# Performance work log

Measured on AMD Instinct MI355X. Metric: run time of the kernel, lower is better.

Reference implementation:

```python
import jax, jax.numpy as jnp
import numpy as np

B, N, HD = 4, 2048, 256
E, T = 4096, 1024
PROPAG_STEPS = 5
ALPHA_MAX = 0.2
LN_EPS = 1e-5


def setup_inputs() -> dict:
    key = jax.random.key(0)
    ks = jax.random.split(key, 16)
    s_in, s_h = (2.0 * HD) ** -0.5, HD ** -0.5
    return {
        "attr_matrix": jax.random.normal(ks[0], (B, N, 1), dtype=jnp.float32),
        "adj_matrix": jax.random.uniform(ks[1], (B, N, N), dtype=jnp.float32),
        # ggnn.linear_i: 1 -> HD
        "W_i": jax.random.normal(ks[2], (HD, 1), dtype=jnp.float32),
        "b_i": jnp.zeros((HD,), dtype=jnp.float32),
        # ggnn.gru: GRUCell(input=2*HD, hidden=HD), torch gate order r,z,n
        "W_ih": jax.random.normal(ks[3], (3 * HD, 2 * HD), dtype=jnp.float32) * s_in,
        "b_ih": jnp.zeros((3 * HD,), dtype=jnp.float32),
        "W_hh": jax.random.normal(ks[4], (3 * HD, HD), dtype=jnp.float32) * s_h,
        "b_hh": jnp.zeros((3 * HD,), dtype=jnp.float32),
        # ggnn.linear_o: HD -> 1
        "W_o": jax.random.normal(ks[5], (1, HD), dtype=jnp.float32) * s_h,
        "b_o": jnp.zeros((1,), dtype=jnp.float32),
        # topo buffers (incidence-like, kept small to mimic sparse +/-1 matrices)
        "B1": jax.random.normal(ks[6], (N, E), dtype=jnp.float32) * 0.02,
        "B2": jax.random.normal(ks[7], (E, T), dtype=jnp.float32) * 0.02,
        # topo trainables
        "proj_W": jax.random.normal(ks[8], (HD, HD), dtype=jnp.float32) * s_h,
        "ln_gamma": jnp.ones((HD,), dtype=jnp.float32),
        "ln_beta": jnp.zeros((HD,), dtype=jnp.float32),
        "alpha_raw": jnp.float32(-2.0),
    }


def _gru_cell(x, h, W_ih, b_ih, W_hh, b_hh):
    # x: [B,N,2H], h: [B,N,H]; torch GRUCell gate order: r, z, n
    gx = jnp.einsum('bni,gi->bng', x, W_ih) + b_ih
    gh = jnp.einsum('bnh,gh->bng', h, W_hh) + b_hh
    xr, xz, xn = jnp.split(gx, 3, axis=-1)
    hr, hz, hn = jnp.split(gh, 3, axis=-1)
    r = jax.nn.sigmoid(xr + hr)
    z = jax.nn.sigmoid(xz + hz)
    n = jnp.tanh(xn + r * hn)
    return (1.0 - z) * n + z * h


def _layernorm(x, gamma, beta):
    mu = jnp.mean(x, axis=-1, keepdims=True)
    var = jnp.mean(jnp.square(x - mu), axis=-1, keepdims=True)
    return (x - mu) * jax.lax.rsqrt(var + LN_EPS) * gamma + beta


def reference(attr_matrix, adj_matrix, W_i, b_i, W_ih, b_ih, W_hh, b_hh,
              W_o, b_o, B1, B2, proj_W, ln_gamma, ln_beta, alpha_raw):
    A_in = adj_matrix                      # [B,N,N]
    A_out = jnp.swapaxes(adj_matrix, -2, -1)
    # linear_i + relu
    h = jax.nn.relu(jnp.einsum('bnc,hc->bnh', attr_matrix, W_i) + b_i)  # [B,N,H]
    # GGNN propagation
    for _ in range(PROPAG_STEPS):
        a_in = jnp.einsum('bnm,bmh->bnh', A_in, h)
        a_out = jnp.einsum('bnm,bmh->bnh', A_out, h)
        h = _gru_cell(jnp.concatenate((a_in, a_out), axis=-1), h,
                      W_ih, b_ih, W_hh, b_hh)
    # topo residual: dH = B1 (L1 (B1^T h)), L1 = B1^T B1 + B2 B2^T
    L1 = B1.T @ B1 + B2 @ B2.T             # [E,E]
    E_feat = jnp.einsum('ne,bnh->beh', B1, h)       # B1^T H
    E_topo = jnp.einsum('ef,bfh->beh', L1, E_feat)
    dH = jnp.einsum('ne,beh->bnh', B1, E_topo)
    dH = _layernorm(jax.nn.relu(jnp.einsum('bnh,oh->bno', dH, proj_W)),
                    ln_gamma, ln_beta)
    alpha = ALPHA_MAX * jax.nn.sigmoid(alpha_raw)
    h = h + alpha * dH
    # linear_o -> [B,N] (squeeze(0) is a no-op for B>1)
    anomaly = (jnp.einsum('bnh,oh->bno', h, W_o) + b_o)[..., 0]
    return anomaly
```

## Files before the change

### kernel.cpp

```cpp
#include <hip/hip_runtime.h>
#include <hip/hip_fp16.h>


typedef __bf16 bf16x8 __attribute__((ext_vector_type(8)));
typedef _Float16 f16x8 __attribute__((ext_vector_type(8)));
typedef float f32x4 __attribute__((ext_vector_type(4)));

#define BM 128
#define BN 128
#define BK 16
#define LO_INV (1.f / 1024.f)

__device__ __forceinline__ unsigned short bf16rne(float x)
{
    unsigned u = __float_as_uint(x);
    return (unsigned short)((u + 0x7FFFu + ((u >> 16) & 1u)) >> 16);
}
__device__ __forceinline__ float bf2f(unsigned short h)
{
    return __uint_as_float((unsigned)h << 16);
}
__device__ __forceinline__ void split2(float x, unsigned short& hi, unsigned short& lo)
{
    hi = bf16rne(x);
    lo = bf16rne(x - bf2f(hi));
}

__device__ __forceinline__ unsigned short f16r(float x)
{
    return __half_as_ushort(__float2half(x));
}
__device__ __forceinline__ float f16f(unsigned short u)
{
    return __half2float(__ushort_as_half(u));
}
__device__ __forceinline__ void splitf(float x, unsigned short& hi, unsigned short& lo)
{
    hi = f16r(x);
    lo = f16r((x - f16f(hi)) * 1024.f);
}

__device__ __forceinline__ void gload_lds16(const unsigned short* g, unsigned short* l)
{
    __builtin_amdgcn_global_load_lds(
        (const __attribute__((address_space(1))) void*)g,
        (__attribute__((address_space(3))) void*)l, 16, 0, 0);
}

__device__ __forceinline__ void stage2(const unsigned short* g, unsigned short* l, int K)
{
    gload_lds16(g, l);
    gload_lds16(g + (size_t)32 * K, l + 2048);
}

template<int SPLIT>
__device__ __forceinline__ void mm_loop64f(
    const unsigned short* ag0, const unsigned short* ag1,
    const unsigned short* bg0, const unsigned short* bg1,
    int K, unsigned short* LDS, int tid,
    f32x4 (&acc0)[2][2], f32x4 (&acc1)[2][2])
{
    constexpr int NT = SPLIT ? 2 : 1;
    constexpr int TSZ = 4096;

    int lane = tid & 63, r16 = lane & 15, g = lane >> 4, s7 = r16 & 7;
    int wv = tid >> 6, wr = wv >> 1, wc = wv & 1;
    int arow = (wr * 32 + r16) * 128;
    int brow = (wc * 32 + r16) * 128;
    unsigned short* lA = LDS + (tid >> 6) * 512;
    unsigned short* lB = LDS + NT * TSZ + (tid >> 6) * 512;
    const char* Ab = (const char*)LDS;
    const char* Bb = (const char*)(LDS + NT * TSZ);

    for (int k0 = 0; k0 < K; k0 += 64) {
        stage2(ag0 + k0, lA, K);
        if constexpr (SPLIT) stage2(ag1 + k0, lA + TSZ, K);
        stage2(bg0 + k0, lB, K);
        if constexpr (SPLIT) stage2(bg1 + k0, lB + TSZ, K);
        __syncthreads();
#pragma unroll
        for (int ks = 0; ks < 2; ++ks) {
            int tt = ((ks * 4 + g) ^ s7) * 16;
            f16x8 a0[2], a1[2], b0[2], b1[2];
#pragma unroll
            for (int mi = 0; mi < 2; ++mi) {
                a0[mi] = *(const f16x8*)(Ab + arow + mi * 2048 + tt);
                if constexpr (SPLIT)
                    a1[mi] = *(const f16x8*)(Ab + TSZ * 2 + arow + mi * 2048 + tt);
            }
#pragma unroll
            for (int ni = 0; ni < 2; ++ni) {
                b0[ni] = *(const f16x8*)(Bb + brow + ni * 2048 + tt);
                if constexpr (SPLIT)
                    b1[ni] = *(const f16x8*)(Bb + TSZ * 2 + brow + ni * 2048 + tt);
            }
#pragma unroll
            for (int mi = 0; mi < 2; ++mi)
#pragma unroll
                for (int ni = 0; ni < 2; ++ni) {
                    if constexpr (SPLIT) {
                        acc1[mi][ni] = __builtin_amdgcn_mfma_f32_16x16x32_f16(
                            a1[mi], b0[ni], acc1[mi][ni], 0, 0, 0);
                        acc1[mi][ni] = __builtin_amdgcn_mfma_f32_16x16x32_f16(
                            a0[mi], b1[ni], acc1[mi][ni], 0, 0, 0);
                    }
                    acc0[mi][ni] = __builtin_amdgcn_mfma_f32_16x16x32_f16(
                        a0[mi], b0[ni], acc0[mi][ni], 0, 0, 0);
                }
        }
        __syncthreads();
    }
}

template<int SPLIT, int OF16>
__global__ __launch_bounds__(256, 2) void mm_f16(
    const unsigned short* __restrict__ Ah, const unsigned short* __restrict__ Al,
    const unsigned short* __restrict__ Bh, const unsigned short* __restrict__ Bl,
    int K, const float* __restrict__ bias, const float* __restrict__ Cacc,
    void* __restrict__ Cout, int ldc)
{
    constexpr int NT = SPLIT ? 2 : 1;
    __shared__ unsigned short LDS[2 * NT * 4096];
    int tid = threadIdx.x;

    unsigned nwg = gridDim.x * gridDim.y;
    unsigned lin = blockIdx.y * gridDim.x + blockIdx.x;
    unsigned wk = ((nwg & 7) == 0) ? (lin & 7) * (nwg >> 3) + (lin >> 3) : lin;
    unsigned bx = wk % gridDim.x, by = wk / gridDim.x;

    int m0 = by * 64, n0 = bx * 64;
    int rp = tid >> 3, sl8 = ((tid & 7) ^ (rp & 7)) * 8;
    const unsigned short* ag0 = Ah + (size_t)(m0 + rp) * K + sl8;
    const unsigned short* ag1 = SPLIT ? Al + (size_t)(m0 + rp) * K + sl8 : nullptr;
    const unsigned short* bg0 = Bh + (size_t)(n0 + rp) * K + sl8;
    const unsigned short* bg1 = SPLIT ? Bl + (size_t)(n0 + rp) * K + sl8 : nullptr;

    f32x4 acc0[2][2], acc1[2][2];
#pragma unroll
    for (int mi = 0; mi < 2; ++mi)
#pragma unroll
        for (int ni = 0; ni < 2; ++ni) {
            acc0[mi][ni] = (f32x4){0.f, 0.f, 0.f, 0.f};
            acc1[mi][ni] = (f32x4){0.f, 0.f, 0.f, 0.f};
        }

    mm_loop64f<SPLIT>(ag0, ag1, bg0, bg1, K, LDS, tid, acc0, acc1);

    int lane = tid & 63, r16 = lane & 15, g = lane >> 4;
    int wv = tid >> 6, wr = wv >> 1, wc = wv & 1;
#pragma unroll
    for (int mi = 0; mi < 2; ++mi) {
#pragma unroll
        for (int ni = 0; ni < 2; ++ni) {
            int col = n0 + wc * 32 + ni * 16 + r16;
            float badd = bias ? bias[col] : 0.f;
#pragma unroll
            for (int j = 0; j < 4; ++j) {
                int row = m0 + wr * 32 + mi * 16 + g * 4 + j;
                float v = acc0[mi][ni][j] + badd;
                if (SPLIT) v += acc1[mi][ni][j] * LO_INV;
                if (Cacc) v += Cacc[(size_t)row * ldc + col];
                if (OF16)
                    ((unsigned short*)Cout)[(size_t)row * ldc + col] = f16r(v);
                else
                    ((float*)Cout)[(size_t)row * ldc + col] = v;
            }
        }
    }
}

__global__ __launch_bounds__(256, 2) void mm_step1f(
    const unsigned short* __restrict__ AhHi, const unsigned short* __restrict__ AhLo,
    const unsigned short* __restrict__ AtHi, const unsigned short* __restrict__ AtLo,
    const unsigned short* __restrict__ hTh, const unsigned short* __restrict__ hTl,
    unsigned short* __restrict__ Xhi, unsigned short* __restrict__ Xlo,
    const unsigned short* __restrict__ hrmh, const unsigned short* __restrict__ hrml,
    const unsigned short* __restrict__ WhhH, const unsigned short* __restrict__ WhhL,
    const float* __restrict__ b_hh, float* __restrict__ ghb)
{
    __shared__ unsigned short LDS[16384];
    int tid = threadIdx.x;
    unsigned bid = blockIdx.x;
    int lane = tid & 63, r16 = lane & 15, g = lane >> 4;
    int wv = tid >> 6, wr = wv >> 1, wc = wv & 1;
    int rp = tid >> 3, sl8 = ((tid & 7) ^ (rp & 7)) * 8;

    f32x4 acc0[2][2], acc1[2][2];
#pragma unroll
    for (int mi = 0; mi < 2; ++mi)
#pragma unroll
        for (int ni = 0; ni < 2; ++ni) {
            acc0[mi][ni] = (f32x4){0.f, 0.f, 0.f, 0.f};
            acc1[mi][ni] = (f32x4){0.f, 0.f, 0.f, 0.f};
        }

    if (bid < 1024) {
        unsigned wk = (bid & 7) * 128 + (bid >> 3);
        unsigned bz = wk >> 7, rem = wk & 127, by = rem >> 2, bx = rem & 3;
        int b = bz >> 1, wio = bz & 1;
        const unsigned short* Ahp = (wio ? AtHi : AhHi) + (size_t)b * 4194304;
        const unsigned short* Alp = (wio ? AtLo : AhLo) + (size_t)b * 4194304;
        size_t boff = (size_t)(b * 256 + bx * 64) * 2048;
        int m0 = by * 64;
        const int K = 2048;
        const unsigned short* ag0 = Ahp + (size_t)(m0 + rp) * K + sl8;
        const unsigned short* ag1 = Alp + (size_t)(m0 + rp) * K + sl8;
        const unsigned short* bg0 = hTh + boff + (size_t)rp * K + sl8;
        const unsigned short* bg1 = hTl + boff + (size_t)rp * K + sl8;

        mm_loop64f<1>(ag0, ag1, bg0, bg1, K, LDS, tid, acc0, acc1);

        float* T = reinterpret_cast<float*>(LDS);
#pragma unroll
        for (int mi = 0; mi < 2; ++mi)
#pragma unroll
            for (int ni = 0; ni < 2; ++ni)
#pragma unroll
                for (int j = 0; j < 4; ++j)
                    T[(wr * 32 + mi * 16 + g * 4 + j) * 68 +
                      wc * 32 + ni * 16 + r16] =
                        acc0[mi][ni][j] + acc1[mi][ni][j] * LO_INV;
        __syncthreads();

        int row = tid >> 2, fq = tid & 3;
        const float* src = T + row * 68 + fq * 16;
        unsigned hw[8], lw[8];
#pragma unroll
        for (int e = 0; e < 8; ++e) {
            unsigned short h0, l0, h1, l1;
            splitf(src[2 * e], h0, l0);
            splitf(src[2 * e + 1], h1, l1);
            hw[e] = (unsigned)h0 | ((unsigned)h1 << 16);
            lw[e] = (unsigned)l0 | ((unsigned)l1 << 16);
        }
        size_t base = ((size_t)(m0 + row) * 4 + b) * 512 + wio * 256 + bx * 64 + fq * 16;
        ((uint4*)(Xhi + base))[0] = (uint4){hw[0], hw[1], hw[2], hw[3]};
        ((uint4*)(Xhi + base))[1] = (uint4){hw[4], hw[5], hw[6], hw[7]};
        ((uint4*)(Xlo + base))[0] = (uint4){lw[0], lw[1], lw[2], lw[3]};
        ((uint4*)(Xlo + base))[1] = (uint4){lw[4], lw[5], lw[6], lw[7]};
    } else {
        unsigned gidx = bid - 1024;
        unsigned by = gidx / 12, bx = gidx % 12;
        int m0 = by * 64, n0 = bx * 64;
        const int K = 256;
        const unsigned short* ag0 = hrmh + (size_t)(m0 + rp) * K + sl8;
        const unsigned short* ag1 = hrml + (size_t)(m0 + rp) * K + sl8;
        const unsigned short* bg0 = WhhH + (size_t)(n0 + rp) * K + sl8;
        const unsigned short* bg1 = WhhL + (size_t)(n0 + rp) * K + sl8;

        mm_loop64f<1>(ag0, ag1, bg0, bg1, K, LDS, tid, acc0, acc1);

#pragma unroll
        for (int mi = 0; mi < 2; ++mi) {
#pragma unroll
            for (int ni = 0; ni < 2; ++ni) {
                int col = n0 + wc * 32 + ni * 16 + r16;
                float badd = b_hh[col];
#pragma unroll
                for (int j = 0; j < 4; ++j) {
                    int row = m0 + wr * 32 + mi * 16 + g * 4 + j;
                    ghb[(size_t)row * 768 + col] =
                        acc0[mi][ni][j] + acc1[mi][ni][j] * LO_INV + badd;
                }
            }
        }
    }
}

__global__ void split_adj16(const float* __restrict__ adj,
                            unsigned short* __restrict__ nhi, unsigned short* __restrict__ nlo,
                            unsigned short* __restrict__ thi, unsigned short* __restrict__ tlo)
{
    __shared__ float t[64][68];
    int z = blockIdx.z;
    const float* src = adj + (size_t)z * 4194304;
    int tx = threadIdx.x & 15, ty = threadIdx.x >> 4;
    int i0 = blockIdx.y * 64, j0 = blockIdx.x * 64;
#pragma unroll
    for (int i = 0; i < 4; ++i) {
        int r = ty * 4 + i;
        float4 v = *(const float4*)(src + (size_t)(i0 + r) * 2048 + j0 + tx * 4);
        ushort4 h, l;
        splitf(v.x, h.x, l.x); splitf(v.y, h.y, l.y);
        splitf(v.z, h.z, l.z); splitf(v.w, h.w, l.w);
        size_t o = (size_t)z * 4194304 + (size_t)(i0 + r) * 2048 + j0 + tx * 4;
        *(ushort4*)(nhi + o) = h; *(ushort4*)(nlo + o) = l;
        t[r][tx * 4 + 0] = v.x; t[r][tx * 4 + 1] = v.y;
        t[r][tx * 4 + 2] = v.z; t[r][tx * 4 + 3] = v.w;
    }
    __syncthreads();
#pragma unroll
    for (int i = 0; i < 4; ++i) {
        int r = ty * 4 + i;
        ushort4 h, l;
        splitf(t[tx * 4 + 0][r], h.x, l.x);
        splitf(t[tx * 4 + 1][r], h.y, l.y);
        splitf(t[tx * 4 + 2][r], h.z, l.z);
        splitf(t[tx * 4 + 3][r], h.w, l.w);
        size_t o = (size_t)z * 4194304 + (size_t)(j0 + r) * 2048 + i0 + tx * 4;
        *(ushort4*)(thi + o) = h; *(ushort4*)(tlo + o) = l;
    }
}

__global__ void split_h16(const float* __restrict__ h,
                          unsigned short* __restrict__ hi, unsigned short* __restrict__ lo,
                          unsigned short* __restrict__ hrmh, unsigned short* __restrict__ hrml)
{
    __shared__ float t[64][68];
    int f0 = blockIdx.x * 64, n0 = blockIdx.y * 64;
    int tx = threadIdx.x & 15, ty = threadIdx.x >> 4;
#pragma unroll
    for (int i = 0; i < 4; ++i) {
        int r = ty * 4 + i;
        float4 v = *(const float4*)(h + (size_t)(n0 + r) * 1024 + f0 + tx * 4);
        t[r][tx * 4 + 0] = v.x; t[r][tx * 4 + 1] = v.y;
        t[r][tx * 4 + 2] = v.z; t[r][tx * 4 + 3] = v.w;
        if (hrmh) {
            ushort4 hh, ll;
            splitf(v.x, hh.x, ll.x); splitf(v.y, hh.y, ll.y);
            splitf(v.z, hh.z, ll.z); splitf(v.w, hh.w, ll.w);
            size_t o = (size_t)(n0 + r) * 1024 + f0 + tx * 4;
            *(ushort4*)(hrmh + o) = hh;
            *(ushort4*)(hrml + o) = ll;
        }
    }
    __syncthreads();
#pragma unroll
    for (int i = 0; i < 4; ++i) {
        int r = ty * 4 + i;
        ushort4 hh, ll;
        splitf(t[tx * 4 + 0][r], hh.x, ll.x);
        splitf(t[tx * 4 + 1][r], hh.y, ll.y);
        splitf(t[tx * 4 + 2][r], hh.z, ll.z);
        splitf(t[tx * 4 + 3][r], hh.w, ll.w);
        size_t o = (size_t)(f0 + r) * 2048 + n0 + tx * 4;
        *(ushort4*)(hi + o) = hh; *(ushort4*)(lo + o) = ll;
    }
}

__global__ void split_t16(const float* __restrict__ in, unsigned short* __restrict__ outN,
                          unsigned short* __restrict__ outT, int R, int C)
{
    __shared__ float t[64][68];
    int i0 = blockIdx.y * 64, j0 = blockIdx.x * 64;
    int tx = threadIdx.x & 15, ty = threadIdx.x >> 4;
#pragma unroll
    for (int i = 0; i < 4; ++i) {
        int r = ty * 4 + i;
        float4 v = *(const float4*)(in + (size_t)(i0 + r) * C + j0 + tx * 4);
        ushort4 hh;
        hh.x = f16r(v.x); hh.y = f16r(v.y);
        hh.z = f16r(v.z); hh.w = f16r(v.w);
        *(ushort4*)(outN + (size_t)(i0 + r) * C + j0 + tx * 4) = hh;
        t[r][tx * 4 + 0] = v.x; t[r][tx * 4 + 1] = v.y;
        t[r][tx * 4 + 2] = v.z; t[r][tx * 4 + 3] = v.w;
    }
    __syncthreads();
#pragma unroll
    for (int i = 0; i < 4; ++i) {
        int r = ty * 4 + i;
        ushort4 hh;
        hh.x = f16r(t[tx * 4 + 0][r]);
        hh.y = f16r(t[tx * 4 + 1][r]);
        hh.z = f16r(t[tx * 4 + 2][r]);
        hh.w = f16r(t[tx * 4 + 3][r]);
        *(ushort4*)(outT + (size_t)(j0 + r) * R + i0 + tx * 4) = hh;
    }
}

__global__ void split_w16(const float* __restrict__ Wih, const float* __restrict__ Whh,
                          const float* __restrict__ pj,
                          unsigned short* __restrict__ WihH, unsigned short* __restrict__ WihL,
                          unsigned short* __restrict__ WhhH, unsigned short* __restrict__ WhhL,
                          unsigned short* __restrict__ pjH)
{
    int i = blockIdx.x * 256 + threadIdx.x;
    if (i < 393216) {
        unsigned short h, l;
        splitf(Wih[i], h, l);
        WihH[i] = h; WihL[i] = l;
    } else if (i < 589824) {
        int j = i - 393216;
        unsigned short h, l;
        splitf(Whh[j], h, l);
        WhhH[j] = h; WhhL[j] = l;
    } else if (i < 655360) {
        int j = i - 589824;
        pjH[j] = f16r(pj[j]);
    }
}

__global__ __launch_bounds__(256, 2) void gemm_f32(
    const float* __restrict__ A, const float* __restrict__ B, float* __restrict__ C,
    int M, int N, int K, int lda, int ldb, int ldc,
    long sA, long sB, long sC,
    const float* __restrict__ bias, int ta, int tb, int accum)
{
    int bz = blockIdx.z;
    int taEff = ta;
    if (ta == 2) {
        int b = bz >> 1, w = bz & 1;
        A += (long)b * sA; B += (long)b * sB; C += (long)b * sC + w * 256;
        taEff = w;
    } else {
        A += (long)bz * sA; B += (long)bz * sB; C += (long)bz * sC;
    }
    int m0 = blockIdx.y * BM, n0 = blockIdx.x * BN;

    __shared__ float As[BK][BM + 4];
    __shared__ float Bs[BK][BN + 4];

    int tid = threadIdx.x;
    int tx = tid & 15, ty = tid >> 4;

    float acc[64];
#pragma unroll
    for (int i = 0; i < 64; ++i) acc[i] = 0.f;

    for (int k0 = 0; k0 < K; k0 += BK) {
        if (!taEff) {
            int m = tid >> 1, kk = (tid & 1) * 8;
            const float* src = A + (long)(m0 + m) * lda + (k0 + kk);
            float4 v0 = *(const float4*)(src);
            float4 v1 = *(const float4*)(src + 4);
            As[kk + 0][m] = v0.x; As[kk + 1][m] = v0.y;
            As[kk + 2][m] = v0.z; As[kk + 3][m] = v0.w;
            As[kk + 4][m] = v1.x; As[kk + 5][m] = v1.y;
            As[kk + 6][m] = v1.z; As[kk + 7][m] = v1.w;
        } else {
            int k = tid >> 4, mm = (tid & 15) * 8;
            const float* src = A + (long)(k0 + k) * lda + (m0 + mm);
            *(float4*)&As[k][mm]     = *(const float4*)(src);
            *(float4*)&As[k][mm + 4] = *(const float4*)(src + 4);
        }
        if (!tb) {
            int k = tid >> 4, nn = (tid & 15) * 8;
            const float* src = B + (long)(k0 + k) * ldb + (n0 + nn);
            *(float4*)&Bs[k][nn]     = *(const float4*)(src);
            *(float4*)&Bs[k][nn + 4] = *(const float4*)(src + 4);
        } else {
            int n = tid >> 1, kk = (tid & 1) * 8;
            const float* src = B + (long)(n0 + n) * ldb + (k0 + kk);
            float4 v0 = *(const float4*)(src);
            float4 v1 = *(const float4*)(src + 4);
            Bs[kk + 0][n] = v0.x; Bs[kk + 1][n] = v0.y;
            Bs[kk + 2][n] = v0.z; Bs[kk + 3][n] = v0.w;
            Bs[kk + 4][n] = v1.x; Bs[kk + 5][n] = v1.y;
            Bs[kk + 6][n] = v1.z; Bs[kk + 7][n] = v1.w;
        }
        __syncthreads();

#pragma unroll
        for (int k = 0; k < BK; ++k) {
            float a[8], b[8];
            *(float4*)&a[0] = *(const float4*)&As[k][ty * 4];
            *(float4*)&a[4] = *(const float4*)&As[k][64 + ty * 4];
            *(float4*)&b[0] = *(const float4*)&Bs[k][tx * 4];
            *(float4*)&b[4] = *(const float4*)&Bs[k][64 + tx * 4];
#pragma unroll
            for (int i = 0; i < 8; ++i)
#pragma unroll
                for (int j = 0; j < 8; ++j)
                    acc[i * 8 + j] += a[i] * b[j];
        }
        __syncthreads();
    }

#pragma unroll
    for (int i = 0; i < 8; ++i) {
        int row = m0 + ((i >> 2) ? 64 : 0) + ty * 4 + (i & 3);
#pragma unroll
        for (int jh = 0; jh < 2; ++jh) {
            int col = n0 + jh * 64 + tx * 4;
            float4 v;
            v.x = acc[i * 8 + jh * 4 + 0];
            v.y = acc[i * 8 + jh * 4 + 1];
            v.z = acc[i * 8 + jh * 4 + 2];
            v.w = acc[i * 8 + jh * 4 + 3];
            if (bias) {
                v.x += bias[col + 0]; v.y += bias[col + 1];
                v.z += bias[col + 2]; v.w += bias[col + 3];
            }
            float* dst = C + (long)row * ldc + col;
            if (accum) {
                float4 o = *(const float4*)dst;
                v.x += o.x; v.y += o.y; v.z += o.z; v.w += o.w;
            }
            *(float4*)dst = v;
        }
    }
}

__global__ void split_adj(const float* __restrict__ adj,
                          unsigned short* __restrict__ nhi, unsigned short* __restrict__ nlo,
                          unsigned short* __restrict__ thi, unsigned short* __restrict__ tlo)
{
    __shared__ float t[64][68];
    int z = blockIdx.z;
    const float* src = adj + (size_t)z * 4194304;
    int tx = threadIdx.x & 15, ty = threadIdx.x >> 4;
    int i0 = blockIdx.y * 64, j0 = blockIdx.x * 64;
#pragma unroll
    for (int i = 0; i < 4; ++i) {
        int r = ty * 4 + i;
        float4 v = *(const float4*)(src + (size_t)(i0 + r) * 2048 + j0 + tx * 4);
        ushort4 h, l;
        split2(v.x, h.x, l.x); split2(v.y, h.y, l.y);
        split2(v.z, h.z, l.z); split2(v.w, h.w, l.w);
        size_t o = (size_t)z * 4194304 + (size_t)(i0 + r) * 2048 + j0 + tx * 4;
        *(ushort4*)(nhi + o) = h; *(ushort4*)(nlo + o) = l;
        t[r][tx * 4 + 0] = v.x; t[r][tx * 4 + 1] = v.y;
        t[r][tx * 4 + 2] = v.z; t[r][tx * 4 + 3] = v.w;
    }
    __syncthreads();
#pragma unroll
    for (int i = 0; i < 4; ++i) {
        int r = ty * 4 + i;
        ushort4 h, l;
        split2(t[tx * 4 + 0][r], h.x, l.x);
        split2(t[tx * 4 + 1][r], h.y, l.y);
        split2(t[tx * 4 + 2][r], h.z, l.z);
        split2(t[tx * 4 + 3][r], h.w, l.w);
        size_t o = (size_t)z * 4194304 + (size_t)(j0 + r) * 2048 + i0 + tx * 4;
        *(ushort4*)(thi + o) = h; *(ushort4*)(tlo + o) = l;
    }
}

__global__ void split_h(const float* __restrict__ h,
                        unsigned short* __restrict__ hi, unsigned short* __restrict__ lo)
{
    __shared__ float t[64][68];
    int f0 = blockIdx.x * 64, n0 = blockIdx.y * 64;
    int tx = threadIdx.x & 15, ty = threadIdx.x >> 4;
#pragma unroll
    for (int i = 0; i < 4; ++i) {
        int r = ty * 4 + i;
        float4 v = *(const float4*)(h + (size_t)(n0 + r) * 1024 + f0 + tx * 4);
        t[r][tx * 4 + 0] = v.x; t[r][tx * 4 + 1] = v.y;
        t[r][tx * 4 + 2] = v.z; t[r][tx * 4 + 3] = v.w;
    }
    __syncthreads();
#pragma unroll
    for (int i = 0; i < 4; ++i) {
        int r = ty * 4 + i;
        ushort4 hh, ll;
        split2(t[tx * 4 + 0][r], hh.x, ll.x);
        split2(t[tx * 4 + 1][r], hh.y, ll.y);
        split2(t[tx * 4 + 2][r], hh.z, ll.z);
        split2(t[tx * 4 + 3][r], hh.w, ll.w);
        size_t o = (size_t)(f0 + r) * 2048 + n0 + tx * 4;
        *(ushort4*)(hi + o) = hh; *(ushort4*)(lo + o) = ll;
    }
}

__global__ __launch_bounds__(256, 3) void adj_mfma(
    const unsigned short* __restrict__ AhHi, const unsigned short* __restrict__ AhLo,
    const unsigned short* __restrict__ AtHi, const unsigned short* __restrict__ AtLo,
    const unsigned short* __restrict__ hTHi, const unsigned short* __restrict__ hTLo,
    float* __restrict__ c0, float* __restrict__ c1, float* __restrict__ c2)
{
    __shared__ unsigned short As[8192];
    __shared__ unsigned short Bs[8192];
    int tid = threadIdx.x;
    int bz = blockIdx.z;
    int region = bz >> 3, bw = bz & 7, b = bw >> 1, w = bw & 1;
    const unsigned short* Abase =
        (region == 2) ? (w ? AtLo : AhLo) : (w ? AtHi : AhHi);
    Abase += (size_t)b * 4194304;
    const unsigned short* Bbase = (region == 1) ? hTLo : hTHi;
    float* Cb = (region == 0) ? c0 : (region == 1 ? c1 : c2);

    int m0 = blockIdx.y * 128;
    int f0 = b * 256 + blockIdx.x * 128;

    int rp = tid >> 3;
    int sl = (tid & 7) ^ (rp & 7);
    const unsigned short* ag = Abase + (size_t)(m0 + rp) * 2048 + sl * 8;
    const unsigned short* bg = Bbase + (size_t)(f0 + rp) * 2048 + sl * 8;
    unsigned short* al = &As[(tid >> 6) * 512];
    unsigned short* bl = &Bs[(tid >> 6) * 512];

    int lane = tid & 63, r16 = lane & 15, g = lane >> 4;
    int wv = tid >> 6, wr = wv >> 1, wc = wv & 1;
    int s7 = r16 & 7;
    int t0 = (g ^ s7) * 16, t1 = ((4 + g) ^ s7) * 16;
    int arow = (wr * 64 + r16) * 128;
    int brow = (wc * 64 + r16) * 128;

    f32x4 acc[4][4];
#pragma unroll
    for (int mi = 0; mi < 4; ++mi)
#pragma unroll
        for (int ni = 0; ni < 4; ++ni)
            acc[mi][ni] = (f32x4){0.f, 0.f, 0.f, 0.f};

    for (int k0 = 0; k0 < 2048; k0 += 64) {
#pragma unroll
        for (int i = 0; i < 4; ++i)
            gload_lds16(ag + k0 + (size_t)i * 65536, al + i * 2048);
#pragma unroll
        for (int i = 0; i < 4; ++i)
            gload_lds16(bg + k0 + (size_t)i * 65536, bl + i * 2048);
        __syncthreads();

#pragma unroll
        for (int ks = 0; ks < 2; ++ks) {
            int tt = ks ? t1 : t0;
            bf16x8 af[4], bf[4];
#pragma unroll
            for (int mi = 0; mi < 4; ++mi)
                af[mi] = *(const bf16x8*)((const char*)As + arow + mi * 2048 + tt);
#pragma unroll
            for (int ni = 0; ni < 4; ++ni)
                bf[ni] = *(const bf16x8*)((const char*)Bs + brow + ni * 2048 + tt);
#pragma unroll
            for (int mi = 0; mi < 4; ++mi)
#pragma unroll
                for (int ni = 0; ni < 4; ++ni)
                    acc[mi][ni] = __builtin_amdgcn_mfma_f32_16x16x32_bf16(
                        af[mi], bf[ni], acc[mi][ni], 0, 0, 0);
        }
        __syncthreads();
    }

    int cbase = b * 512 + w * 256 + blockIdx.x * 128 + wc * 64;
#pragma unroll
    for (int mi = 0; mi < 4; ++mi) {
        int row = m0 + wr * 64 + mi * 16 + g * 4;
#pragma unroll
        for (int ni = 0; ni < 4; ++ni) {
            int col = cbase + ni * 16 + r16;
            float* dst = Cb + (size_t)row * 2048 + col;
#pragma unroll
            for (int j = 0; j < 4; ++j) dst[(size_t)j * 2048] = acc[mi][ni][j];
        }
    }
}

__global__ void reduce3(float4* __restrict__ x, const float4* __restrict__ p,
                        const float4* __restrict__ q)
{
    int i = blockIdx.x * 256 + threadIdx.x;
    float4 a = x[i], b = p[i], c = q[i];
    a.x += b.x + c.x; a.y += b.y + c.y; a.z += b.z + c.z; a.w += b.w + c.w;
    x[i] = a;
}

__global__ void init_h(const float* __restrict__ attr, const float* __restrict__ W_i,
                       const float* __restrict__ b_i, float* __restrict__ h)
{
    int n = blockIdx.x, b = blockIdx.y, t = threadIdx.x;
    float a = attr[b * 2048 + n];
    h[(long)n * 1024 + b * 256 + t] = fmaxf(a * W_i[t] + b_i[t], 0.f);
}

__global__ void gru_ew(const float* __restrict__ gx, const float* __restrict__ gh,
                       float* __restrict__ h)
{
    int n = blockIdx.x, b = blockIdx.y, t = threadIdx.x;
    long row = ((long)n * 4 + b) * 768;
    float xr = gx[row + t], xz = gx[row + 256 + t], xn = gx[row + 512 + t];
    float hr = gh[row + t], hz = gh[row + 256 + t], hn = gh[row + 512 + t];
    float r = 1.f / (1.f + __expf(-(xr + hr)));
    float z = 1.f / (1.f + __expf(-(xz + hz)));
    float nn = tanhf(xn + r * hn);
    long hi = (long)n * 1024 + b * 256 + t;
    float ho = h[hi];
    h[hi] = (1.f - z) * nn + z * ho;
}

__global__ void ln_out(const float* __restrict__ dP, const float* __restrict__ gamma,
                       const float* __restrict__ beta, const float* __restrict__ araw,
                       const float* __restrict__ h, const float* __restrict__ W_o,
                       const float* __restrict__ b_o, float* __restrict__ out)
{
    int n = blockIdx.x, b = blockIdx.y, t = threadIdx.x;
    long row = ((long)n * 4 + b) * 256;
    float v = fmaxf(dP[row + t], 0.f);
    float s = v, s2 = v * v;
#pragma unroll
    for (int o = 1; o < 64; o <<= 1) { s += __shfl_xor(s, o); s2 += __shfl_xor(s2, o); }
    __shared__ float red[8];
    int w = t >> 6, lane = t & 63;
    if (lane == 0) { red[w] = s; red[4 + w] = s2; }
    __syncthreads();
    float S  = red[0] + red[1] + red[2] + red[3];
    float S2 = red[4] + red[5] + red[6] + red[7];
    float mu = S * (1.f / 256.f);
    float var = S2 * (1.f / 256.f) - mu * mu;
    float rs = rsqrtf(var + 1e-5f);
    float alpha = 0.2f / (1.f + __expf(-araw[0]));
    float y = h[(long)n * 1024 + b * 256 + t] +
              alpha * ((v - mu) * rs * gamma[t] + beta[t]);
    float d = y * W_o[t];
#pragma unroll
    for (int o = 1; o < 64; o <<= 1) d += __shfl_xor(d, o);
    __syncthreads();
    if (lane == 0) red[w] = d;
    __syncthreads();
    if (t == 0) out[(long)b * 2048 + n] = red[0] + red[1] + red[2] + red[3] + b_o[0];
}

__global__ void ln_residual(const float* __restrict__ dP, const float* __restrict__ gamma,
                            const float* __restrict__ beta, const float* __restrict__ araw,
                            float* __restrict__ h)
{
    int n = blockIdx.x, b = blockIdx.y, t = threadIdx.x;
    long row = ((long)n * 4 + b) * 256;
    float v = fmaxf(dP[row + t], 0.f);
    float s = v, s2 = v * v;
#pragma unroll
    for (int o = 1; o < 64; o <<= 1) { s += __shfl_xor(s, o); s2 += __shfl_xor(s2, o); }
    __shared__ float red[8];
    int w = t >> 6, lane = t & 63;
    if (lane == 0) { red[w] = s; red[4 + w] = s2; }
    __syncthreads();
    float S  = red[0] + red[1] + red[2] + red[3];
    float S2 = red[4] + red[5] + red[6] + red[7];
    float mu = S * (1.f / 256.f);
    float var = S2 * (1.f / 256.f) - mu * mu;
    float rs = rsqrtf(var + 1e-5f);
    float alpha = 0.2f / (1.f + __expf(-araw[0]));
    long hi = (long)n * 1024 + b * 256 + t;
    h[hi] += alpha * ((v - mu) * rs * gamma[t] + beta[t]);
}

__global__ void out_kernel(const float* __restrict__ h, const float* __restrict__ W_o,
                           const float* __restrict__ b_o, float* __restrict__ out)
{
    int t = threadIdx.x;
    int w = t >> 6, lane = t & 63;
    int row = blockIdx.x * 4 + w;
    int n = row >> 2, b = row & 3;
    const float* hp = h + (long)n * 1024 + b * 256;
    float s = 0.f;
#pragma unroll
    for (int i = 0; i < 4; ++i) { int c = i * 64 + lane; s += hp[c] * W_o[c]; }
#pragma unroll
    for (int o = 1; o < 64; o <<= 1) s += __shfl_xor(s, o);
    if (lane == 0) out[(long)b * 2048 + n] = s + b_o[0];
}

extern "C" void kernel_launch(void* const* d_in, const int* in_sizes, int n_in,
                              void* d_out, int out_size, void* d_ws, size_t ws_size,
                              hipStream_t stream)
{
    (void)in_sizes; (void)n_in; (void)out_size;
    const float* attr  = (const float*)d_in[0];
    const float* adj   = (const float*)d_in[1];
    const float* W_i   = (const float*)d_in[2];
    const float* b_i   = (const float*)d_in[3];
    const float* W_ih  = (const float*)d_in[4];
    const float* b_ih  = (const float*)d_in[5];
    const float* W_hh  = (const float*)d_in[6];
    const float* b_hh  = (const float*)d_in[7];
    const float* W_o   = (const float*)d_in[8];
    const float* b_o   = (const float*)d_in[9];
    const float* B1    = (const float*)d_in[10];
    const float* B2    = (const float*)d_in[11];
    const float* projW = (const float*)d_in[12];
    const float* gamma = (const float*)d_in[13];
    const float* beta  = (const float*)d_in[14];
    const float* araw  = (const float*)d_in[15];
    float* out = (float*)d_out;

    char* wsb = (char*)d_ws;
    dim3 blk(256);

    const size_t REQ1 = 0xD400000;
    const size_t REQ2 = 0xD000000;

    if (ws_size >= REQ1) {
        float* hbuf = (float*)(wsb);
        float* gxb  = (float*)(wsb + 0x0800000);
        unsigned short* hrmh = (unsigned short*)(wsb + 0x0800000);
        unsigned short* hrml = (unsigned short*)(wsb + 0x0C00000);
        unsigned short* hTh  = (unsigned short*)(wsb + 0x1800000);
        unsigned short* hTl  = (unsigned short*)(wsb + 0x1C00000);
        float* ghb  = (float*)(wsb + 0x2000000);
        unsigned short* Xhi = (unsigned short*)(wsb + 0x3800000);
        unsigned short* Xlo = (unsigned short*)(wsb + 0x4000000);
        unsigned short* Wih_h = (unsigned short*)(wsb + 0x5000000);
        unsigned short* Wih_l = (unsigned short*)(wsb + 0x50C0000);
        unsigned short* Whh_h = (unsigned short*)(wsb + 0x5240000);
        unsigned short* Whh_l = (unsigned short*)(wsb + 0x52A0000);
        unsigned short* pjh   = (unsigned short*)(wsb + 0x5300000);
        char* R1 = wsb + 0x5400000;
        unsigned short* AhHi = (unsigned short*)(R1);
        unsigned short* AhLo = (unsigned short*)(R1 + 0x2000000);
        unsigned short* AtHi = (unsigned short*)(R1 + 0x4000000);
        unsigned short* AtLo = (unsigned short*)(R1 + 0x6000000);
        unsigned short* B1h = (unsigned short*)(R1);
        unsigned short* B1T = (unsigned short*)(R1 + 0x1000000);
        unsigned short* B2h = (unsigned short*)(R1 + 0x2000000);
        unsigned short* B2T = (unsigned short*)(R1 + 0x2800000);
        unsigned short* uTb = (unsigned short*)(R1 + 0x3000000);
        unsigned short* pTb = (unsigned short*)(R1 + 0x3800000);
        unsigned short* rTb = (unsigned short*)(R1 + 0x3C00000);
        unsigned short* qTb = (unsigned short*)(R1 + 0x3E00000);
        float* qTf = gxb;
        unsigned short* dHb = (unsigned short*)(wsb + 0x1800000);
        float* dPb = ghb;

        init_h<<<dim3(2048, 4), blk, 0, stream>>>(attr, W_i, b_i, hbuf);
        split_adj16<<<dim3(32, 32, 4), blk, 0, stream>>>(adj, AhHi, AhLo, AtHi, AtLo);
        split_w16<<<dim3(2560), blk, 0, stream>>>(W_ih, W_hh, projW,
            Wih_h, Wih_l, Whh_h, Whh_l, pjh);

        for (int step = 0; step < 5; ++step) {
            split_h16<<<dim3(16, 32), blk, 0, stream>>>(hbuf, hTh, hTl, hrmh, hrml);
            mm_step1f<<<dim3(2560), blk, 0, stream>>>(
                AhHi, AhLo, AtHi, AtLo, hTh, hTl, Xhi, Xlo,
                hrmh, hrml, Whh_h, Whh_l, b_hh, ghb);
            mm_f16<1, 0><<<dim3(12, 128), blk, 0, stream>>>(
                Xhi, Xlo, Wih_h, Wih_l, 512, b_ih, nullptr, gxb, 768);
            gru_ew<<<dim3(2048, 4), blk, 0, stream>>>(gxb, ghb, hbuf);
        }

        split_h16<<<dim3(16, 32), blk, 0, stream>>>(hbuf, hTh, hTl, nullptr, nullptr);
        split_t16<<<dim3(64, 32), blk, 0, stream>>>(B1, B1h, B1T, 2048, 4096);
        split_t16<<<dim3(16, 64), blk, 0, stream>>>(B2, B2h, B2T, 4096, 1024);
        mm_f16<0, 1><<<dim3(64, 16), blk, 0, stream>>>(
            hTh, nullptr, B1T, nullptr, 2048, nullptr, nullptr, uTb, 4096);
        mm_f16<0, 1><<<dim3(32, 16), blk, 0, stream>>>(
            uTb, nullptr, B1h, nullptr, 4096, nullptr, nullptr, pTb, 2048);
        mm_f16<0, 1><<<dim3(16, 16), blk, 0, stream>>>(
            uTb, nullptr, B2T, nullptr, 4096, nullptr, nullptr, rTb, 1024);
        mm_f16<0, 0><<<dim3(64, 16), blk, 0, stream>>>(
            pTb, nullptr, B1T, nullptr, 2048, nullptr, nullptr, qTf, 4096);
        mm_f16<0, 1><<<dim3(64, 16), blk, 0, stream>>>(
            rTb, nullptr, B2h, nullptr, 1024, nullptr, qTf, qTb, 4096);
        mm_f16<0, 1><<<dim3(16, 32), blk, 0, stream>>>(
            B1h, nullptr, qTb, nullptr, 4096, nullptr, nullptr, dHb, 1024);
        mm_f16<0, 0><<<dim3(4, 128), blk, 0, stream>>>(
            dHb, nullptr, pjh, nullptr, 256, nullptr, nullptr, dPb, 256);

        ln_out<<<dim3(2048, 4), blk, 0, stream>>>(dPb, gamma, beta, araw,
                                                  hbuf, W_o, b_o, out);
        return;
    }

    float* hbuf = (float*)(wsb);
    float* xbuf = (float*)(wsb + 0x800000);
    float* gxb  = (float*)(wsb + 0x1800000);
    float* ghb  = (float*)(wsb + 0x3000000);
    unsigned short* AhHi = (unsigned short*)(wsb + 0x4800000);
    unsigned short* AhLo = (unsigned short*)(wsb + 0x6800000);
    unsigned short* AtHi = (unsigned short*)(wsb + 0x8800000);
    unsigned short* AtLo = (unsigned short*)(wsb + 0xA800000);
    unsigned short* hTHi = (unsigned short*)(wsb + 0xC800000);
    unsigned short* hTLo = (unsigned short*)(wsb + 0xCC00000);

    float* ub  = xbuf;
    float* pb  = gxb;
    float* qb  = gxb + (1 << 21);
    float* rb  = ghb;
    float* dHr = ghb + (1 << 20);
    float* dPb = ghb + 3 * (1 << 20);

    bool mfma_path = (ws_size >= REQ2);

    init_h<<<dim3(2048, 4), blk, 0, stream>>>(attr, W_i, b_i, hbuf);

    if (mfma_path)
        split_adj<<<dim3(32, 32, 4), blk, 0, stream>>>(adj, AhHi, AhLo, AtHi, AtLo);

    for (int step = 0; step < 5; ++step) {
        if (mfma_path) {
            split_h<<<dim3(16, 32), blk, 0, stream>>>(hbuf, hTHi, hTLo);
            adj_mfma<<<dim3(2, 16, 24), blk, 0, stream>>>(
                AhHi, AhLo, AtHi, AtLo, hTHi, hTLo, xbuf, gxb, ghb);
            reduce3<<<dim3(4096), blk, 0, stream>>>(
                (float4*)xbuf, (const float4*)gxb, (const float4*)ghb);
        } else {
            gemm_f32<<<dim3(2, 16, 8), blk, 0, stream>>>(
                adj, hbuf, xbuf, 2048, 256, 2048, 2048, 1024, 2048,
                (long)2048 * 2048, 256, 512, nullptr, 2, 0, 0);
        }
        gemm_f32<<<dim3(6, 64, 1), blk, 0, stream>>>(
            xbuf, W_ih, gxb, 8192, 768, 512, 512, 512, 768,
            0, 0, 0, b_ih, 0, 1, 0);
        gemm_f32<<<dim3(6, 64, 1), blk, 0, stream>>>(
            hbuf, W_hh, ghb, 8192, 768, 256, 256, 256, 768,
            0, 0, 0, b_hh, 0, 1, 0);
        gru_ew<<<dim3(2048, 4), blk, 0, stream>>>(gxb, ghb, hbuf);
    }

    gemm_f32<<<dim3(8, 32, 1), blk, 0, stream>>>(
        B1, hbuf, ub, 4096, 1024, 2048, 4096, 1024, 1024, 0, 0, 0, nullptr, 1, 0, 0);
    gemm_f32<<<dim3(8, 16, 1), blk, 0, stream>>>(
        B1, ub, pb, 2048, 1024, 4096, 4096, 1024, 1024, 0, 0, 0, nullptr, 0, 0, 0);
    gemm_f32<<<dim3(8, 32, 1), blk, 0, stream>>>(
        B1, pb, qb, 4096, 1024, 2048, 4096, 1024, 1024, 0, 0, 0, nullptr, 1, 0, 0);
    gemm_f32<<<dim3(8, 8, 1), blk, 0, stream>>>(
        B2, ub, rb, 1024, 1024, 4096, 1024, 1024, 1024, 0, 0, 0, nullptr, 1, 0, 0);
    gemm_f32<<<dim3(8, 32, 1), blk, 0, stream>>>(
        B2, rb, qb, 4096, 1024, 1024, 1024, 1024, 1024, 0, 0, 0, nullptr, 0, 0, 1);
    gemm_f32<<<dim3(8, 16, 1), blk, 0, stream>>>(
        B1, qb, dHr, 2048, 1024, 4096, 4096, 1024, 1024, 0, 0, 0, nullptr, 0, 0, 0);
    gemm_f32<<<dim3(2, 64, 1), blk, 0, stream>>>(
        dHr, projW, dPb, 8192, 256, 256, 256, 256, 256, 0, 0, 0, nullptr, 0, 1, 0);

    ln_residual<<<dim3(2048, 4), blk, 0, stream>>>(dPb, gamma, beta, araw, hbuf);
    out_kernel<<<dim3(2048), blk, 0, stream>>>(hbuf, W_o, b_o, out);
}
```

Before: 856.9 us.

## Fuse input-gate GEMM with GRU elementwise update into one kernel

```diff
diff --git a/kernel.cpp b/kernel.cpp
--- a/kernel.cpp
+++ b/kernel.cpp
@@ -164,6 +164,115 @@
                     ((unsigned short*)Cout)[(size_t)row * ldc + col] = f16r(v);
                 else
                     ((float*)Cout)[(size_t)row * ldc + col] = v;
+            }
+        }
+    }
+}
+
+__global__ __launch_bounds__(256, 2) void gxgru(
+    const unsigned short* __restrict__ Xhi, const unsigned short* __restrict__ Xlo,
+    const unsigned short* __restrict__ WihH, const unsigned short* __restrict__ WihL,
+    const float* __restrict__ b_ih, const float* __restrict__ ghb,
+    float* __restrict__ h)
+{
+    __shared__ unsigned short LDS[32768];
+    int tid = threadIdx.x;
+
+    unsigned lin = blockIdx.y * 4 + blockIdx.x;
+    unsigned wk = (lin & 7) * 64 + (lin >> 3);
+    unsigned tb = wk & 3, by = wk >> 2;
+
+    int m0 = by * 64;
+    const int K = 512;
+    int rp = tid >> 3, sl8 = ((tid & 7) ^ (rp & 7)) * 8;
+    const unsigned short* ag0 = Xhi + (size_t)(m0 + rp) * K + sl8;
+    const unsigned short* ag1 = Xlo + (size_t)(m0 + rp) * K + sl8;
+    const unsigned short* bh0 = WihH + (size_t)(tb * 192 + rp) * K + sl8;
+    const unsigned short* bl0 = WihL + (size_t)(tb * 192 + rp) * K + sl8;
+
+    int lane = tid & 63, r16 = lane & 15, lg = lane >> 4, s7 = r16 & 7;
+    int wv = tid >> 6, wr = wv >> 1, wc = wv & 1;
+    int arow = (wr * 32 + r16) * 128;
+    int brow = (wc * 32 + r16) * 128;
+    unsigned short* lA = LDS + (tid >> 6) * 512;
+    unsigned short* lB = LDS + 8192 + (tid >> 6) * 512;
+
+    f32x4 acc0[3][2][2], acc1[3][2][2];
+#pragma unroll
+    for (int g = 0; g < 3; ++g)
+#pragma unroll
+        for (int mi = 0; mi < 2; ++mi)
+#pragma unroll
+            for (int ni = 0; ni < 2; ++ni) {
+                acc0[g][mi][ni] = (f32x4){0.f, 0.f, 0.f, 0.f};
+                acc1[g][mi][ni] = (f32x4){0.f, 0.f, 0.f, 0.f};
+            }
+
+    for (int k0 = 0; k0 < K; k0 += 64) {
+        stage2(ag0 + k0, lA, K);
+        stage2(ag1 + k0, lA + 4096, K);
+#pragma unroll
+        for (int g = 0; g < 3; ++g) {
+            stage2(bh0 + (size_t)(g * 64) * K + k0, lB + g * 4096, K);
+            stage2(bl0 + (size_t)(g * 64) * K + k0, lB + 12288 + g * 4096, K);
+        }
+        __syncthreads();
+#pragma unroll
+        for (int ks = 0; ks < 2; ++ks) {
+            int tt = ((ks * 4 + lg) ^ s7) * 16;
+            f16x8 a0[2], a1[2];
+#pragma unroll
+            for (int mi = 0; mi < 2; ++mi) {
+                a0[mi] = *(const f16x8*)((const char*)LDS + arow + mi * 2048 + tt);
+                a1[mi] = *(const f16x8*)((const char*)LDS + 8192 + arow + mi * 2048 + tt);
+            }
+#pragma unroll
+            for (int g = 0; g < 3; ++g) {
+                f16x8 b0[2], b1[2];
+#pragma unroll
+                for (int ni = 0; ni < 2; ++ni) {
+                    b0[ni] = *(const f16x8*)((const char*)LDS + 16384 + g * 8192 +
+                                             brow + ni * 2048 + tt);
+                    b1[ni] = *(const f16x8*)((const char*)LDS + 40960 + g * 8192 +
+                                             brow + ni * 2048 + tt);
+                }
+#pragma unroll
+                for (int mi = 0; mi < 2; ++mi)
+#pragma unroll
+                    for (int ni = 0; ni < 2; ++ni) {
+                        acc1[g][mi][ni] = __builtin_amdgcn_mfma_f32_16x16x32_f16(
+                            a1[mi], b0[ni], acc1[g][mi][ni], 0, 0, 0);
+                        acc1[g][mi][ni] = __builtin_amdgcn_mfma_f32_16x16x32_f16(
+                            a0[mi], b1[ni], acc1[g][mi][ni], 0, 0, 0);
+                        acc0[g][mi][ni] = __builtin_amdgcn_mfma_f32_16x16x32_f16(
+                            a0[mi], b0[ni], acc0[g][mi][ni], 0, 0, 0);
+                    }
+            }
+        }
+        __syncthreads();
+    }
+
+#pragma unroll
+    for (int mi = 0; mi < 2; ++mi) {
+#pragma unroll
+        for (int ni = 0; ni < 2; ++ni) {
+            int t = tb * 64 + wc * 32 + ni * 16 + r16;
+            float br = b_ih[t], bz = b_ih[256 + t], bn = b_ih[512 + t];
+#pragma unroll
+            for (int j = 0; j < 4; ++j) {
+                int row = m0 + wr * 32 + mi * 16 + lg * 4 + j;
+                float xr = acc0[0][mi][ni][j] + acc1[0][mi][ni][j] * LO_INV + br;
+                float xz = acc0[1][mi][ni][j] + acc1[1][mi][ni][j] * LO_INV + bz;
+                float xn = acc0[2][mi][ni][j] + acc1[2][mi][ni][j] * LO_INV + bn;
+                size_t grow = (size_t)row * 768;
+                float hr = ghb[grow + t];
+                float hz = ghb[grow + 256 + t];
+                float hn = ghb[grow + 512 + t];
+                float r = 1.f / (1.f + __expf(-(xr + hr)));
+                float z = 1.f / (1.f + __expf(-(xz + hz)));
+                float nn = tanhf(xn + r * hn);
+                size_t hix = (size_t)row * 256 + t;
+                h[hix] = (1.f - z) * nn + z * h[hix];
             }
         }
     }
@@ -376,9 +485,12 @@
 {
     int i = blockIdx.x * 256 + threadIdx.x;
     if (i < 393216) {
+        int row = i >> 9, col = i & 511;
+        int g = row >> 8, t = row & 255;
+        int nrow = (t >> 6) * 192 + g * 64 + (t & 63);
         unsigned short h, l;
         splitf(Wih[i], h, l);
-        WihH[i] = h; WihL[i] = l;
+        WihH[nrow * 512 + col] = h; WihL[nrow * 512 + col] = l;
     } else if (i < 589824) {
         int j = i - 393216;
         unsigned short h, l;
@@ -812,9 +924,8 @@
             mm_step1f<<<dim3(2560), blk, 0, stream>>>(
                 AhHi, AhLo, AtHi, AtLo, hTh, hTl, Xhi, Xlo,
                 hrmh, hrml, Whh_h, Whh_l, b_hh, ghb);
-            mm_f16<1, 0><<<dim3(12, 128), blk, 0, stream>>>(
-                Xhi, Xlo, Wih_h, Wih_l, 512, b_ih, nullptr, gxb, 768);
-            gru_ew<<<dim3(2048, 4), blk, 0, stream>>>(gxb, ghb, hbuf);
+            gxgru<<<dim3(4, 128), blk, 0, stream>>>(
+                Xhi, Xlo, Wih_h, Wih_l, b_ih, ghb, hbuf);
         }
 
         split_h16<<<dim3(16, 32), blk, 0, stream>>>(hbuf, hTh, hTl, nullptr, nullptr);
```

Result: faster. 780.9 us (-8.9%).
